# Kernel tuning notes

Measured on AMD Instinct MI355X. Metric: run time of the kernel, lower is better.

## Reference

```python
import jax, jax.numpy as jnp
import numpy as np

B, K, L, D = 64, 64, 128, 128  # batch, top_k, max_length, embedding_dimension
H = 2 * D                      # MLP input size (context || gathered entity)
N_HIDDEN = 6                   # Linear(H,H) layers with Tanh (dropout is eval no-op)


def setup_inputs() -> dict:
    key = jax.random.key(0)
    k0, k1, k2 = jax.random.split(key, 3)
    context = jax.random.normal(k0, (B, K, 2, L, D), dtype=jnp.float32)
    Ws = jax.random.normal(k1, (N_HIDDEN, H, H), dtype=jnp.float32) * 0.05
    bs = jnp.zeros((N_HIDDEN, H), dtype=jnp.float32)
    W_out = jax.random.normal(k2, (H,), dtype=jnp.float32) * 0.05
    b_out = jnp.zeros((), dtype=jnp.float32)
    return {"context": context, "Ws": Ws, "bs": bs, "W_out": W_out, "b_out": b_out}


def reference(context, Ws, bs, W_out, b_out):
    ctx = context[:, :, 0]  # [B,K,L,D]
    ent = context[:, :, 1]  # [B,K,L,D]
    cn = jnp.linalg.norm(ctx, axis=-1, keepdims=True)  # [B,K,L,1]
    en = jnp.linalg.norm(ent, axis=-1, keepdims=True)  # [B,K,L,1]
    # cosine-similarity matrix between context rows and entity rows
    sim = jnp.einsum("bkld,bkmd->bklm", ctx, ent) / (cn * jnp.swapaxes(en, -1, -2))
    ctx_n = ctx / cn
    ent_n = ent / en
    idx = jnp.argmax(sim, axis=-1)  # [B,K,L] top-1 entity row per context row
    gathered = jnp.take_along_axis(
        ent_n, jnp.broadcast_to(idx[..., None], ent_n.shape), axis=2
    )  # [B,K,L,D]
    # stack(...,-2) then flatten(start_dim=-2) == concat along feature dim
    x = jnp.concatenate([ctx_n, gathered], axis=-1)  # [B,K,L,2D]
    for i in range(N_HIDDEN):
        x = jnp.tanh(x @ Ws[i].T + bs[i])
    out = x @ W_out + b_out  # [B,K,L]
    return jnp.sum(out, axis=-1)  # [B,K] (sum over L then squeeze)
```

## Files before the change

kernel.cpp:

```cpp
#include <hip/hip_runtime.h>

#define HID4(r,c4) ((r)*64 + ((((c4) ^ ((r)&15))) << 2))
#define XIDX(r,c)  ((r)*256 + (((((c)>>3) ^ ((r)&7))) << 3) + ((c)&7))

typedef _Float16 half_t;
typedef __attribute__((ext_vector_type(8))) _Float16 f16x8;
typedef __attribute__((ext_vector_type(4))) float f32x4;

__device__ __forceinline__ float tanh_fast(float x){
    float e = __expf(2.0f * x);
    return 1.0f - 2.0f / (e + 1.0f);
}

__device__ __forceinline__ f16x8 cvt8(float4 a, float4 b){
    f16x8 r;
    r[0]=(half_t)a.x; r[1]=(half_t)a.y; r[2]=(half_t)a.z; r[3]=(half_t)a.w;
    r[4]=(half_t)b.x; r[5]=(half_t)b.y; r[6]=(half_t)b.z; r[7]=(half_t)b.w;
    return r;
}

__device__ __forceinline__ void gload16(const void* g, void* l){
    __builtin_amdgcn_global_load_lds((const __attribute__((address_space(1))) unsigned int*)g,
                                     (__attribute__((address_space(3))) unsigned int*)l, 16, 0, 0);
}

__global__ __launch_bounds__(512, 4)
void fused_mlp_som(const float* __restrict__ ctx_in,
                   const float* __restrict__ Ws,
                   const float* __restrict__ bs,
                   const float* __restrict__ Wout,
                   const float* __restrict__ bout,
                   float* __restrict__ out)
{
    extern __shared__ char smem[];
    float* S0     = (float*)smem;
    float* S1     = S0 + 128*64;
    float* inv_cn = S1 + 128*64;
    float* inv_en = inv_cn + 128;
    int*   idxm   = (int*)(inv_en + 128);
    float* redbuf = (float*)(idxm + 128);
    half_t* xf    = (half_t*)smem;

    const int tid  = threadIdx.x;
    const int lane = tid & 63;
    const int bk   = blockIdx.x;
    const int wid  = tid >> 6;

    const float*  gctx = ctx_in + (size_t)bk * 32768;
    const float*  gent = gctx + 16384;
    const float4* gc4  = (const float4*)gctx;
    const float4* ge4  = (const float4*)gent;

    const int isEnt = tid >> 8;
    const int hf    = tid & 1;
    const int nr    = (tid >> 1) & 127;
    float ns = 0.f;

    const int ti = tid >> 5;
    const int tj = tid & 31;
    const int l0 = ti * 8;
    float acc[8][4];
    #pragma unroll
    for (int i = 0; i < 8; ++i)
        #pragma unroll
        for (int j = 0; j < 4; ++j) acc[i][j] = 0.f;

    const int lr = lane >> 4;
    const int lp = lane & 15;

    #pragma unroll 1
    for (int h = 0; h < 2; ++h){
        if (h) __syncthreads();
        #pragma unroll
        for (int it = 0; it < 4; ++it){
            const int rb  = 16*wid + 4*it;
            const int rsw = 4*it + lr;
            const int gsw = lp ^ rsw;
            gload16(gc4 + (rb + lr)*32 + 16*h + gsw, (char*)smem + rb*256);
            gload16(ge4 + (rb + lr)*32 + 16*h + gsw, (char*)smem + 32768 + rb*256);
        }
        __syncthreads();
        if (hf == h){
            const float* T = isEnt ? S1 : S0;
            #pragma unroll
            for (int u = 0; u < 16; ++u){
                float4 v = *(const float4*)&T[HID4(nr, u)];
                ns = fmaf(v.x, v.x, ns); ns = fmaf(v.y, v.y, ns);
                ns = fmaf(v.z, v.z, ns); ns = fmaf(v.w, v.w, ns);
            }
        }
        for (int kk = 0; kk < 16; ++kk){
            float4 e0 = *(const float4*)&S1[HID4(tj     , kk)];
            float4 e1 = *(const float4*)&S1[HID4(tj + 32, kk)];
            float4 e2 = *(const float4*)&S1[HID4(tj + 64, kk)];
            float4 e3 = *(const float4*)&S1[HID4(tj + 96, kk)];
            #pragma unroll
            for (int i = 0; i < 8; ++i){
                float4 a = *(const float4*)&S0[HID4(l0+i, kk)];
                acc[i][0] = fmaf(a.x,e0.x,acc[i][0]); acc[i][0] = fmaf(a.y,e0.y,acc[i][0]);
                acc[i][0] = fmaf(a.z,e0.z,acc[i][0]); acc[i][0] = fmaf(a.w,e0.w,acc[i][0]);
                acc[i][1] = fmaf(a.x,e1.x,acc[i][1]); acc[i][1] = fmaf(a.y,e1.y,acc[i][1]);
                acc[i][1] = fmaf(a.z,e1.z,acc[i][1]); acc[i][1] = fmaf(a.w,e1.w,acc[i][1]);
                acc[i][2] = fmaf(a.x,e2.x,acc[i][2]); acc[i][2] = fmaf(a.y,e2.y,acc[i][2]);
                acc[i][2] = fmaf(a.z,e2.z,acc[i][2]); acc[i][2] = fmaf(a.w,e2.w,acc[i][2]);
                acc[i][3] = fmaf(a.x,e3.x,acc[i][3]); acc[i][3] = fmaf(a.y,e3.y,acc[i][3]);
                acc[i][3] = fmaf(a.z,e3.z,acc[i][3]); acc[i][3] = fmaf(a.w,e3.w,acc[i][3]);
            }
        }
    }

    ns += __shfl_xor(ns, 1);
    if (hf == 0){
        float inv = 1.0f / sqrtf(ns);
        if (isEnt) inv_en[nr] = inv; else inv_cn[nr] = inv;
    }
    __syncthreads();

    #pragma unroll
    for (int i = 0; i < 8; ++i){
        float best = -1e38f; int bi = 0;
        #pragma unroll
        for (int j = 0; j < 4; ++j){
            int m = tj + 32*j;
            float v = acc[i][j] * inv_en[m];
            if (v > best || (v == best && m < bi)){ best = v; bi = m; }
        }
        #pragma unroll
        for (int s = 1; s < 32; s <<= 1){
            float ov = __shfl_xor(best, s);
            int   oi = __shfl_xor(bi,   s);
            if (ov > best || (ov == best && oi < bi)){ best = ov; bi = oi; }
        }
        if (tj == 0) idxm[l0 + i] = bi;
    }
    __syncthreads();

    {
        const int t  = tid & 255;
        const int l  = t >> 1;
        const int hb = t & 1;
        const float4* src;
        float sc;
        int c0;
        if (tid < 256){ src = (const float4*)(gctx + l*128 + 64*hb); sc = inv_cn[l]; c0 = 64*hb; }
        else { int mi = idxm[l]; src = (const float4*)(gent + mi*128 + 64*hb); sc = inv_en[mi]; c0 = 128 + 64*hb; }
        #pragma unroll
        for (int u = 0; u < 8; ++u){
            float4 va = src[2*u];
            float4 vb = src[2*u+1];
            f16x8 hv;
            hv[0]=(half_t)(va.x*sc); hv[1]=(half_t)(va.y*sc); hv[2]=(half_t)(va.z*sc); hv[3]=(half_t)(va.w*sc);
            hv[4]=(half_t)(vb.x*sc); hv[5]=(half_t)(vb.y*sc); hv[6]=(half_t)(vb.z*sc); hv[7]=(half_t)(vb.w*sc);
            int c = c0 + 8*u;
            *(f16x8*)&xf[l*256 + ((((c>>3) ^ (l&7))) << 3)] = hv;
        }
    }
    __syncthreads();

    const int lan15 = lane & 15;
    const int lq    = lane >> 4;
    const int n0    = 32*wid + lan15;
    const int n1    = n0 + 16;
    const int bno0  = n0 * 256;
    const int bno1  = n1 * 256;
    const int kb    = 8*lq;
    const int aBase = lan15*256;

    #pragma unroll 1
    for (int layer = 0; layer < 6; ++layer){
        const float* WsL = Ws + layer*65536;

        f32x4 mac[8][2];
        #pragma unroll
        for (int mt = 0; mt < 8; ++mt){
            mac[mt][0] = (f32x4){0.f,0.f,0.f,0.f};
            mac[mt][1] = (f32x4){0.f,0.f,0.f,0.f};
        }

        #pragma unroll 1
        for (int ks = 0; ks < 8; ++ks){
            const int aoff = (((4*ks + lq) ^ (lan15 & 7)) << 3);
            const int kk   = 32*ks + kb;
            f16x8 b0, b1;
            {
                float4 qa = *(const float4*)&WsL[bno0 + kk];
                float4 qb = *(const float4*)&WsL[bno0 + kk + 4];
                b0 = cvt8(qa, qb);
            }
            __builtin_amdgcn_sched_barrier(0);
            {
                float4 qc = *(const float4*)&WsL[bno1 + kk];
                float4 qd = *(const float4*)&WsL[bno1 + kk + 4];
                b1 = cvt8(qc, qd);
            }
            __builtin_amdgcn_sched_barrier(0);
            #pragma unroll
            for (int bt = 0; bt < 4; ++bt){
                f16x8 a0 = *(const f16x8*)&xf[aBase + (2*bt  )*4096 + aoff];
                f16x8 a1 = *(const f16x8*)&xf[aBase + (2*bt+1)*4096 + aoff];
                mac[2*bt  ][0] = __builtin_amdgcn_mfma_f32_16x16x32_f16(a0, b0, mac[2*bt  ][0], 0,0,0);
                mac[2*bt  ][1] = __builtin_amdgcn_mfma_f32_16x16x32_f16(a0, b1, mac[2*bt  ][1], 0,0,0);
                mac[2*bt+1][0] = __builtin_amdgcn_mfma_f32_16x16x32_f16(a1, b0, mac[2*bt+1][0], 0,0,0);
                mac[2*bt+1][1] = __builtin_amdgcn_mfma_f32_16x16x32_f16(a1, b1, mac[2*bt+1][1], 0,0,0);
                __builtin_amdgcn_sched_barrier(0);
            }
        }
        __syncthreads();

        if (layer < 5){
            float bias0 = bs[layer*256 + n0];
            float bias1 = bs[layer*256 + n1];
            #pragma unroll
            for (int mt = 0; mt < 8; ++mt){
                #pragma unroll
                for (int r = 0; r < 4; ++r){
                    int row = 16*mt + 4*lq + r;
                    xf[XIDX(row, n0)] = (half_t)tanh_fast(mac[mt][0][r] + bias0);
                    xf[XIDX(row, n1)] = (half_t)tanh_fast(mac[mt][1][r] + bias1);
                }
            }
            __syncthreads();
        } else {
            float bias0 = bs[5*256 + n0];
            float bias1 = bs[5*256 + n1];
            float w0 = Wout[n0];
            float w1 = Wout[n1];
            float part = 0.f;
            #pragma unroll
            for (int mt = 0; mt < 8; ++mt){
                #pragma unroll
                for (int r = 0; r < 4; ++r){
                    part = fmaf(tanh_fast(mac[mt][0][r] + bias0), w0, part);
                    part = fmaf(tanh_fast(mac[mt][1][r] + bias1), w1, part);
                }
            }
            #pragma unroll
            for (int s = 1; s < 64; s <<= 1) part += __shfl_xor(part, s);
            if (lane == 0) redbuf[wid] = part;
            __syncthreads();
            if (tid == 0){
                float s = 0.f;
                #pragma unroll
                for (int i = 0; i < 8; ++i) s += redbuf[i];
                out[bk] = s + 128.0f * bout[0];
            }
        }
    }
}

extern "C" void kernel_launch(void* const* d_in, const int* in_sizes, int n_in,
                              void* d_out, int out_size, void* d_ws, size_t ws_size,
                              hipStream_t stream)
{
    (void)in_sizes; (void)n_in; (void)out_size; (void)d_ws; (void)ws_size;
    const float* ctx  = (const float*)d_in[0];
    const float* Ws   = (const float*)d_in[1];
    const float* bs   = (const float*)d_in[2];
    const float* Wout = (const float*)d_in[3];
    const float* bout = (const float*)d_in[4];
    float* out = (float*)d_out;

    const int smem_bytes = 128*64*4*2 + 128*4 + 128*4 + 128*4 + 8*4;
    hipFuncSetAttribute(reinterpret_cast<const void*>(fused_mlp_som),
                        hipFuncAttributeMaxDynamicSharedMemorySize, smem_bytes);
    fused_mlp_som<<<dim3(4096), dim3(512), smem_bytes, stream>>>(ctx, Ws, bs, Wout, bout, out);
}
```

Before: 1.326 ms.

## Retile MLP GEMM warps to 2x4 grid with 64x64 per-wave tiles

Changes the per-wave output tile from 128 rows x 32 columns to 64 rows x 64 columns, arranging 8 waves in a 2x4 grid. Each wave now converts four weight fragments from global fp32 per k-step instead of two, while reading half as many activation fragments from LDS. This cuts LDS activation reads and balances A/B reuse, but doubles the per-wave global weight loads and fp16 conversions, which may raise L2 traffic.

```diff
diff --git a/kernel.cpp b/kernel.cpp
--- a/kernel.cpp
+++ b/kernel.cpp
@@ -159,81 +159,85 @@
 
     const int lan15 = lane & 15;
     const int lq    = lane >> 4;
-    const int n0    = 32*wid + lan15;
-    const int n1    = n0 + 16;
-    const int bno0  = n0 * 256;
-    const int bno1  = n1 * 256;
+    const int wm    = wid >> 2;
+    const int wn    = wid & 3;
     const int kb    = 8*lq;
-    const int aBase = lan15*256;
+    const int aBase = (64*wm + lan15)*256;
+    int bno[4], ncol[4];
+    #pragma unroll
+    for (int nf = 0; nf < 4; ++nf){
+        ncol[nf] = 64*wn + 16*nf + lan15;
+        bno[nf]  = ncol[nf] * 256;
+    }
 
     #pragma unroll 1
     for (int layer = 0; layer < 6; ++layer){
         const float* WsL = Ws + layer*65536;
 
-        f32x4 mac[8][2];
-        #pragma unroll
-        for (int mt = 0; mt < 8; ++mt){
-            mac[mt][0] = (f32x4){0.f,0.f,0.f,0.f};
-            mac[mt][1] = (f32x4){0.f,0.f,0.f,0.f};
-        }
+        f32x4 mac[4][4];
+        #pragma unroll
+        for (int mt = 0; mt < 4; ++mt)
+            #pragma unroll
+            for (int nf = 0; nf < 4; ++nf)
+                mac[mt][nf] = (f32x4){0.f,0.f,0.f,0.f};
 
         #pragma unroll 1
         for (int ks = 0; ks < 8; ++ks){
             const int aoff = (((4*ks + lq) ^ (lan15 & 7)) << 3);
             const int kk   = 32*ks + kb;
-            f16x8 b0, b1;
-            {
-                float4 qa = *(const float4*)&WsL[bno0 + kk];
-                float4 qb = *(const float4*)&WsL[bno0 + kk + 4];
-                b0 = cvt8(qa, qb);
-            }
-            __builtin_amdgcn_sched_barrier(0);
-            {
-                float4 qc = *(const float4*)&WsL[bno1 + kk];
-                float4 qd = *(const float4*)&WsL[bno1 + kk + 4];
-                b1 = cvt8(qc, qd);
-            }
-            __builtin_amdgcn_sched_barrier(0);
-            #pragma unroll
-            for (int bt = 0; bt < 4; ++bt){
+            f16x8 b[4];
+            #pragma unroll
+            for (int nf = 0; nf < 4; ++nf){
+                float4 qa = *(const float4*)&WsL[bno[nf] + kk];
+                float4 qb = *(const float4*)&WsL[bno[nf] + kk + 4];
+                b[nf] = cvt8(qa, qb);
+                __builtin_amdgcn_sched_barrier(0);
+            }
+            #pragma unroll
+            for (int bt = 0; bt < 2; ++bt){
                 f16x8 a0 = *(const f16x8*)&xf[aBase + (2*bt  )*4096 + aoff];
                 f16x8 a1 = *(const f16x8*)&xf[aBase + (2*bt+1)*4096 + aoff];
-                mac[2*bt  ][0] = __builtin_amdgcn_mfma_f32_16x16x32_f16(a0, b0, mac[2*bt  ][0], 0,0,0);
-                mac[2*bt  ][1] = __builtin_amdgcn_mfma_f32_16x16x32_f16(a0, b1, mac[2*bt  ][1], 0,0,0);
-                mac[2*bt+1][0] = __builtin_amdgcn_mfma_f32_16x16x32_f16(a1, b0, mac[2*bt+1][0], 0,0,0);
-                mac[2*bt+1][1] = __builtin_amdgcn_mfma_f32_16x16x32_f16(a1, b1, mac[2*bt+1][1], 0,0,0);
+                #pragma unroll
+                for (int nf = 0; nf < 4; ++nf){
+                    mac[2*bt  ][nf] = __builtin_amdgcn_mfma_f32_16x16x32_f16(a0, b[nf], mac[2*bt  ][nf], 0,0,0);
+                    mac[2*bt+1][nf] = __builtin_amdgcn_mfma_f32_16x16x32_f16(a1, b[nf], mac[2*bt+1][nf], 0,0,0);
+                }
                 __builtin_amdgcn_sched_barrier(0);
             }
         }
         __syncthreads();
 
         if (layer < 5){
-            float bias0 = bs[layer*256 + n0];
-            float bias1 = bs[layer*256 + n1];
-            #pragma unroll
-            for (int mt = 0; mt < 8; ++mt){
-                #pragma unroll
-                for (int r = 0; r < 4; ++r){
-                    int row = 16*mt + 4*lq + r;
-                    xf[XIDX(row, n0)] = (half_t)tanh_fast(mac[mt][0][r] + bias0);
-                    xf[XIDX(row, n1)] = (half_t)tanh_fast(mac[mt][1][r] + bias1);
+            float bias[4];
+            #pragma unroll
+            for (int nf = 0; nf < 4; ++nf) bias[nf] = bs[layer*256 + ncol[nf]];
+            #pragma unroll
+            for (int mt = 0; mt < 4; ++mt){
+                #pragma unroll
+                for (int nf = 0; nf < 4; ++nf){
+                    #pragma unroll
+                    for (int r = 0; r < 4; ++r){
+                        int row = 64*wm + 16*mt + 4*lq + r;
+                        xf[XIDX(row, ncol[nf])] = (half_t)tanh_fast(mac[mt][nf][r] + bias[nf]);
+                    }
                 }
             }
             __syncthreads();
         } else {
-            float bias0 = bs[5*256 + n0];
-            float bias1 = bs[5*256 + n1];
-            float w0 = Wout[n0];
-            float w1 = Wout[n1];
+            float bias[4], w[4];
+            #pragma unroll
+            for (int nf = 0; nf < 4; ++nf){
+                bias[nf] = bs[5*256 + ncol[nf]];
+                w[nf]    = Wout[ncol[nf]];
+            }
             float part = 0.f;
             #pragma unroll
-            for (int mt = 0; mt < 8; ++mt){
-                #pragma unroll
-                for (int r = 0; r < 4; ++r){
-                    part = fmaf(tanh_fast(mac[mt][0][r] + bias0), w0, part);
-                    part = fmaf(tanh_fast(mac[mt][1][r] + bias1), w1, part);
-                }
-            }
+            for (int mt = 0; mt < 4; ++mt)
+                #pragma unroll
+                for (int nf = 0; nf < 4; ++nf)
+                    #pragma unroll
+                    for (int r = 0; r < 4; ++r)
+                        part = fmaf(tanh_fast(mac[mt][nf][r] + bias[nf]), w[nf], part);
             #pragma unroll
             for (int s = 1; s < 64; s <<= 1) part += __shfl_xor(part, s);
             if (lane == 0) redbuf[wid] = part;
```

After: 2.167 ms. 63.3% more time.
